# Kernel tuning notes

Hardware: AMD Instinct MI355X
Metric: run time of the kernel (lower is better)

Reference implementation:

```python
import jax, jax.numpy as jnp
import numpy as np

B, N, NODE_DIM = 64, 64, 192
H = 256          # node_hidden_dim
PDIM = 64        # property_embedding_dim
NUM_EDGE_TYPE = 5
T = 4            # message-passing rounds
E = 16384        # total edges (flattened batched graph)
E_SEL = 65536    # selected candidate pairs


def setup_inputs() -> dict:
    key = jax.random.key(0)
    ks = jax.random.split(key, 24)
    def g(k, shape, scale=0.05):
        return jax.random.normal(k, shape, dtype=jnp.float32) * scale
    inp = {
        "x": jax.random.normal(ks[0], (B, N, NODE_DIM), dtype=jnp.float32),
        "edge_index": jax.random.randint(ks[1], (2, E), 0, B * N, dtype=jnp.int32),
        "edge_attr": jax.random.uniform(ks[2], (E, NUM_EDGE_TYPE), dtype=jnp.float32),
        "props": jax.random.normal(ks[3], (B, 1), dtype=jnp.float32),
        "sel_b": jax.random.randint(ks[4], (E_SEL,), 0, B, dtype=jnp.int32),
        "sel_i": jax.random.randint(ks[5], (E_SEL,), 0, N, dtype=jnp.int32),
        "sel_j": jax.random.randint(ks[6], (E_SEL,), 0, N, dtype=jnp.int32),
        "golden_edge": jax.random.randint(ks[7], (E_SEL,), 0, NUM_EDGE_TYPE, dtype=jnp.int32),
        # parameters
        "W_prop": g(ks[8], (1, PDIM)), "b_prop": jnp.zeros((PDIM,), jnp.float32),
        "W_in": g(ks[9], (NODE_DIM, H)), "b_in": jnp.zeros((H,), jnp.float32),
        "W_msg": g(ks[10], (H + NUM_EDGE_TYPE, H)), "b_msg": jnp.zeros((H,), jnp.float32),
        "W_upd": g(ks[11], (2 * H, H)), "b_upd": jnp.zeros((H,), jnp.float32),
        "W_add": g(ks[12], (H + PDIM, H)), "b_add": jnp.zeros((H,), jnp.float32),
        "W1": g(ks[13], (2 * H, H)), "b1": jnp.zeros((H,), jnp.float32),
        "W2": g(ks[14], (H, H)), "b2": jnp.zeros((H,), jnp.float32),
        "W3": g(ks[15], (H, 2 * H)), "b3": jnp.zeros((2 * H,), jnp.float32),
        "W_out": g(ks[16], (2 * H, NUM_EDGE_TYPE)), "b_out": jnp.zeros((NUM_EDGE_TYPE,), jnp.float32),
    }
    return inp


def reference(x, edge_index, edge_attr, props, sel_b, sel_i, sel_j, golden_edge,
              W_prop, b_prop, W_in, b_in, W_msg, b_msg, W_upd, b_upd,
              W_add, b_add, W1, b1, W2, b2, W3, b3, W_out, b_out):
    BN = B * N
    node_x = x.reshape(BN, NODE_DIM)
    src, dst = edge_index[0], edge_index[1]

    # --- GNN node embedding (t rounds of message passing, opaque Encoder.embed_node) ---
    h = jax.nn.relu(node_x @ W_in + b_in)                       # [BN, H]
    for _ in range(T):
        msg_in = jnp.concatenate([h[src], edge_attr], axis=-1)  # [E, H+num_edge_type]
        msg = jax.nn.relu(msg_in @ W_msg + b_msg)               # [E, H]
        agg = jax.ops.segment_sum(msg, dst, num_segments=BN)    # [BN, H]
        h = jax.nn.relu(jnp.concatenate([h, agg], axis=-1) @ W_upd + b_upd)

    node_emb = h.reshape(B, N, H)

    # --- property conditioning + addition linear ---
    prop = props @ W_prop + b_prop                               # [B, PDIM]
    propp = jnp.broadcast_to(prop[:, None, :], (B, N, PDIM))
    node_embg = jnp.concatenate([node_emb, propp], axis=-1) @ W_add + b_add  # [B, N, H]

    # --- gather selected (src, dst) pairs directly (equiv. to repeat_interleave + boolean mask) ---
    flat = node_embg.reshape(BN, H)
    src_e = flat[sel_b * N + sel_i]                              # [E_SEL, H]
    dst_e = flat[sel_b * N + sel_j]                              # [E_SEL, H]
    pair = jnp.concatenate([src_e, dst_e], axis=-1)              # [E_SEL, 2H]

    # --- edge predictor MLP (3 layers, ReLU between) + output linear ---
    h1 = jax.nn.relu(pair @ W1 + b1)
    h2 = jax.nn.relu(h1 @ W2 + b2)
    h3 = h2 @ W3 + b3
    logits = h3 @ W_out + b_out                                  # [E_SEL, num_edge_type]

    # --- cross entropy (mean) ---
    logp = jax.nn.log_softmax(logits, axis=-1)
    loss = -jnp.mean(jnp.take_along_axis(logp, golden_edge[:, None].astype(jnp.int32), axis=-1))
    return loss
```

## Files before the change

### kernel.cpp

```cpp
#include <hip/hip_runtime.h>
#include <math.h>

#define BN 4096
#define N_PER_B 64
#define NE 16384
#define NSEL 65536
#define NET 5
#define PD 64
#define H1STR 260
#define FSTR 264
#define PTILES 2

typedef float f32x4 __attribute__((ext_vector_type(4)));
typedef float f32x16 __attribute__((ext_vector_type(16)));
typedef short short8 __attribute__((ext_vector_type(8)));
typedef short short4v __attribute__((ext_vector_type(4)));

__device__ __forceinline__ unsigned short f2bf(float f) {
    unsigned int u = __builtin_bit_cast(unsigned int, f);
    u += 0x7fff + ((u >> 16) & 1);
    return (unsigned short)(u >> 16);
}
__device__ __forceinline__ float bf_lo(unsigned int u) {
    return __builtin_bit_cast(float, u << 16);
}
__device__ __forceinline__ float bf_hi(unsigned int u) {
    return __builtin_bit_cast(float, u & 0xffff0000u);
}
__device__ __forceinline__ unsigned int pack2(float a, float b) {
    return (unsigned)f2bf(a) | ((unsigned)f2bf(b) << 16);
}
__device__ __forceinline__ short8 ld_frag(const unsigned short* p) {
    const short4v lo = *(const short4v*)(p);
    const short4v hi = *(const short4v*)(p + 4);
    return __builtin_shufflevector(lo, hi, 0, 1, 2, 3, 4, 5, 6, 7);
}
__device__ __forceinline__ unsigned int addrelu2(unsigned int a, unsigned int b, unsigned int c) {
    const float lo = fmaxf(bf_lo(a) + bf_lo(b) + bf_lo(c), 0.f);
    const float hi = fmaxf(bf_hi(a) + bf_hi(b) + bf_hi(c), 0.f);
    return pack2(lo, hi);
}

__global__ __launch_bounds__(256) void khist_rank(const int* __restrict__ eidx,
                                                  int* __restrict__ deg,
                                                  int* __restrict__ rank)
{
    const int e = blockIdx.x * 256 + threadIdx.x;
    rank[e] = atomicAdd(&deg[eidx[NE + e]], 1);
}

__global__ __launch_bounds__(256) void k_pre(
    const float* __restrict__ W_in, const float* __restrict__ W_msg,
    const float* __restrict__ W_upd, const float* __restrict__ W_add,
    const float* __restrict__ W1, const float* __restrict__ W2,
    const float* __restrict__ W3, const float* __restrict__ b3,
    const float* __restrict__ W_out, const float* __restrict__ b_out,
    const float* __restrict__ props, const float* __restrict__ W_prop,
    const float* __restrict__ b_prop, const float* __restrict__ b_add,
    const float* __restrict__ b_msg, const float* __restrict__ eattr,
    unsigned short* __restrict__ wbf, unsigned short* __restrict__ WfT,
    float* __restrict__ bfv, float* __restrict__ prop_add,
    unsigned short* __restrict__ ETc, float* __restrict__ out,
    int* __restrict__ deg)
{
    __shared__ __align__(16) char smem[16704];
    const int blk = blockIdx.x;
    const int tid = threadIdx.x;

    if (blk < 16) deg[blk * 256 + tid] = 0;
    if (blk == 0 && tid == 0) out[0] = 0.f;

    if (blk < 128) {
        float (*s)[65] = (float(*)[65])smem;
        const int wsel = blk >> 4;
        const int sub = blk & 15;
        const float* src; unsigned short* dst; int K = 256;
        switch (wsel) {
            case 0: src = W_in;              dst = wbf;                         K = 192; break;
            case 1: src = W_msg;             dst = wbf + 49152;                 break;
            case 2: src = W_upd;             dst = wbf + 49152 + 65536;         break;
            case 3: src = W_upd + 256 * 256; dst = wbf + 49152 + 2 * 65536;     break;
            case 4: src = W_add;             dst = wbf + 49152 + 3 * 65536;     break;
            case 5: src = W1;                dst = wbf + 49152 + 4 * 65536;     break;
            case 6: src = W1 + 256 * 256;    dst = wbf + 49152 + 5 * 65536;     break;
            default: src = W2;               dst = wbf + 49152 + 6 * 65536;     break;
        }
        const int k0 = (sub >> 2) * 64;
        const int n0 = (sub & 3) * 64;
        if (k0 >= K) return;
        const int tn = tid & 63;
        const int tg = tid >> 6;
        #pragma unroll
        for (int i = 0; i < 16; ++i) {
            const int kk = tg * 16 + i;
            s[kk][tn] = src[(size_t)(k0 + kk) * 256 + n0 + tn];
        }
        __syncthreads();
        #pragma unroll
        for (int i = 0; i < 16; ++i) {
            const int nn = tg * 16 + i;
            dst[(size_t)(n0 + nn) * K + k0 + tn] = f2bf(s[tn][nn]);
        }
    } else if (blk < 192) {
        const int b = blk - 128;
        const float pv = props[b];
        float acc = b_add[tid];
        for (int p = 0; p < PD; ++p) {
            const float e = fmaf(pv, W_prop[p], b_prop[p]);
            acc = fmaf(e, W_add[(256 + p) * 256 + tid], acc);
        }
        prop_add[b * 256 + tid] = acc;
    } else if (blk < 449) {
        float* part = (float*)smem;
        const int cb = blk - 192;
        float acc[NET] = {0.f, 0.f, 0.f, 0.f, 0.f};
        #pragma unroll
        for (int rep = 0; rep < 2; ++rep) {
            const int j = rep * 256 + tid;
            const float wv = (cb < 256) ? W3[(size_t)cb * 512 + j] : b3[j];
            #pragma unroll
            for (int t = 0; t < NET; ++t) acc[t] = fmaf(wv, W_out[j * NET + t], acc[t]);
        }
        #pragma unroll
        for (int t = 0; t < NET; ++t)
            for (int off = 32; off >= 1; off >>= 1) acc[t] += __shfl_down(acc[t], off);
        if ((tid & 63) == 0) {
            #pragma unroll
            for (int t = 0; t < NET; ++t) part[(tid >> 6) * NET + t] = acc[t];
        }
        __syncthreads();
        if (tid == 0) {
            float s[NET];
            #pragma unroll
            for (int t = 0; t < NET; ++t)
                s[t] = part[t] + part[NET + t] + part[2 * NET + t] + part[3 * NET + t];
            if (cb < 256) {
                #pragma unroll
                for (int t = 0; t < NET; ++t) WfT[t * 256 + cb] = f2bf(s[t]);
                #pragma unroll
                for (int t = NET; t < 16; ++t) WfT[t * 256 + cb] = 0;
            } else {
                #pragma unroll
                for (int t = 0; t < NET; ++t) bfv[t] = s[t] + b_out[t];
            }
        }
    } else {
        float* ea = (float*)smem;
        const int eb = (blk - 449) * 128;
        if (tid < 160)
            *(float4*)&ea[tid * 4] = *(const float4*)(eattr + (size_t)eb * 5 + tid * 4);
        __syncthreads();
        const float* Wme = W_msg + 256 * 256;
        const float w0 = Wme[0 * 256 + tid];
        const float w1 = Wme[1 * 256 + tid];
        const float w2 = Wme[2 * 256 + tid];
        const float w3 = Wme[3 * 256 + tid];
        const float w4 = Wme[4 * 256 + tid];
        const float bm = b_msg[tid];
        for (int i = 0; i < 128; ++i) {
            const float* a = ea + i * 5;
            float v = bm;
            v = fmaf(a[0], w0, v); v = fmaf(a[1], w1, v); v = fmaf(a[2], w2, v);
            v = fmaf(a[3], w3, v); v = fmaf(a[4], w4, v);
            ETc[(size_t)(eb + i) * 256 + tid] = f2bf(v);
        }
    }
}

__global__ __launch_bounds__(1024) void fstep(
    const float* __restrict__ x, const unsigned short* __restrict__ hbuf,
    const unsigned short* __restrict__ Pin, const unsigned short* __restrict__ ETc,
    const int* __restrict__ row_start, const int* __restrict__ srcs,
    const unsigned short* __restrict__ WaT, const unsigned short* __restrict__ WbT,
    const float* __restrict__ bias1,
    const unsigned short* __restrict__ Wp2T, const float* __restrict__ prop_add,
    const unsigned short* __restrict__ W1aT, const unsigned short* __restrict__ W1bT,
    unsigned short* __restrict__ hout, unsigned short* __restrict__ out1,
    unsigned short* __restrict__ out2, int mode,
    const int* __restrict__ eidx, const int* __restrict__ deg,
    const int* __restrict__ rank, int* __restrict__ srcs_w,
    int* __restrict__ row_start_w)
{
    __shared__ __align__(16) char smemb[4 * 16 * FSTR * 2];
    __shared__ int sEdge[256];
    unsigned short* Hg  = (unsigned short*)(smemb);
    unsigned short* Ag  = (unsigned short*)(smemb + 8448);
    unsigned short* Hs  = (unsigned short*)(smemb + 16896);
    unsigned short* H2s = (unsigned short*)(smemb + 25344);
    const int tid = threadIdx.x;

    if (mode == 0 && blockIdx.x >= 256) {
        int* sdeg = (int*)smemb;
        int* ssum = (int*)(smemb + 16384);
        const int t4 = tid * 4;
        const int4 v = *(const int4*)(deg + t4);
        const int l1 = v.x, l2 = v.x + v.y, l3 = v.x + v.y + v.z;
        ssum[tid] = l3 + v.w;
        __syncthreads();
        for (int off = 1; off < 1024; off <<= 1) {
            const int vv = ssum[tid];
            const int add = (tid >= off) ? ssum[tid - off] : 0;
            __syncthreads();
            ssum[tid] = vv + add;
            __syncthreads();
        }
        const int offset = (tid == 0) ? 0 : ssum[tid - 1];
        int4 rs;
        rs.x = offset; rs.y = offset + l1; rs.z = offset + l2; rs.w = offset + l3;
        *(int4*)(sdeg + t4) = rs;
        if (blockIdx.x == 256) {
            *(int4*)(row_start_w + t4) = rs;
            if (tid == 1023) row_start_w[4096] = NE;
        }
        __syncthreads();
        if (tid < 256) {
            const int e = (blockIdx.x - 256) * 256 + tid;
            const int d = eidx[NE + e];
            srcs_w[sdeg[d] + rank[e]] = eidx[e] | (e << 12);
        }
        return;
    }

    const int w = tid >> 6;
    const int lane = tid & 63;
    const int q = lane >> 4;
    const int tx = lane & 15;
    const int m0 = blockIdx.x * 16;
    const int col = w * 16 + tx;

    if (mode != 0) {
        {
            const int r = tid >> 6;
            const int c4 = (tid & 63) * 4;
            *(uint2*)(Hg + r * FSTR + c4) =
                *(const uint2*)(hbuf + (size_t)(m0 + r) * 256 + c4);
        }
        const int beg0 = row_start[m0];
        const int nE = row_start[m0 + 16] - beg0;
        const bool useLds = (nE <= 256);
        if (useLds && tid < nE) sEdge[tid] = srcs[beg0 + tid];
        __syncthreads();
        const int* ep = useLds ? (const int*)sEdge : srcs;
        const int ebias = useLds ? beg0 : 0;
        {
            const int node = m0 + w;
            const int beg = row_start[node] - ebias;
            const int end = row_start[node + 1] - ebias;
            const int c = lane * 4;
            float a0 = 0.f, a1 = 0.f, a2 = 0.f, a3 = 0.f;
            int idx = beg;
            for (; idx + 3 < end; idx += 4) {
                const int k0 = ep[idx],     k1 = ep[idx + 1];
                const int k2 = ep[idx + 2], k3 = ep[idx + 3];
                const uint2 p0 = *(const uint2*)(Pin + (size_t)(k0 & 4095) * 256 + c);
                const uint2 p1 = *(const uint2*)(Pin + (size_t)(k1 & 4095) * 256 + c);
                const uint2 p2 = *(const uint2*)(Pin + (size_t)(k2 & 4095) * 256 + c);
                const uint2 p3 = *(const uint2*)(Pin + (size_t)(k3 & 4095) * 256 + c);
                const uint2 e0 = *(const uint2*)(ETc + (size_t)(k0 >> 12) * 256 + c);
                const uint2 e1 = *(const uint2*)(ETc + (size_t)(k1 >> 12) * 256 + c);
                const uint2 e2 = *(const uint2*)(ETc + (size_t)(k2 >> 12) * 256 + c);
                const uint2 e3 = *(const uint2*)(ETc + (size_t)(k3 >> 12) * 256 + c);
                a0 += fmaxf(bf_lo(p0.x) + bf_lo(e0.x), 0.f) + fmaxf(bf_lo(p1.x) + bf_lo(e1.x), 0.f)
                    + fmaxf(bf_lo(p2.x) + bf_lo(e2.x), 0.f) + fmaxf(bf_lo(p3.x) + bf_lo(e3.x), 0.f);
                a1 += fmaxf(bf_hi(p0.x) + bf_hi(e0.x), 0.f) + fmaxf(bf_hi(p1.x) + bf_hi(e1.x), 0.f)
                    + fmaxf(bf_hi(p2.x) + bf_hi(e2.x), 0.f) + fmaxf(bf_hi(p3.x) + bf_hi(e3.x), 0.f);
                a2 += fmaxf(bf_lo(p0.y) + bf_lo(e0.y), 0.f) + fmaxf(bf_lo(p1.y) + bf_lo(e1.y), 0.f)
                    + fmaxf(bf_lo(p2.y) + bf_lo(e2.y), 0.f) + fmaxf(bf_lo(p3.y) + bf_lo(e3.y), 0.f);
                a3 += fmaxf(bf_hi(p0.y) + bf_hi(e0.y), 0.f) + fmaxf(bf_hi(p1.y) + bf_hi(e1.y), 0.f)
                    + fmaxf(bf_hi(p2.y) + bf_hi(e2.y), 0.f) + fmaxf(bf_hi(p3.y) + bf_hi(e3.y), 0.f);
            }
            for (; idx < end; ++idx) {
                const int pk = ep[idx];
                const uint2 pu = *(const uint2*)(Pin + (size_t)(pk & 4095) * 256 + c);
                const uint2 eu = *(const uint2*)(ETc + (size_t)(pk >> 12) * 256 + c);
                a0 += fmaxf(bf_lo(pu.x) + bf_lo(eu.x), 0.f);
                a1 += fmaxf(bf_hi(pu.x) + bf_hi(eu.x), 0.f);
                a2 += fmaxf(bf_lo(pu.y) + bf_lo(eu.y), 0.f);
                a3 += fmaxf(bf_hi(pu.y) + bf_hi(eu.y), 0.f);
            }
            uint2 o; o.x = pack2(a0, a1); o.y = pack2(a2, a3);
            *(uint2*)(Ag + w * FSTR + c) = o;
        }
        __syncthreads();
    }

    f32x4 acc = (f32x4)0.f;
    if (mode == 0) {
        #pragma unroll
        for (int s = 0; s < 6; ++s) {
            const int k0 = s * 32;
            const float* ap = x + (size_t)(m0 + tx) * 192 + k0 + q * 8;
            const float4 v0 = *(const float4*)ap;
            const float4 v1 = *(const float4*)(ap + 4);
            short8 af;
            af[0] = (short)f2bf(v0.x); af[1] = (short)f2bf(v0.y);
            af[2] = (short)f2bf(v0.z); af[3] = (short)f2bf(v0.w);
            af[4] = (short)f2bf(v1.x); af[5] = (short)f2bf(v1.y);
            af[6] = (short)f2bf(v1.z); af[7] = (short)f2bf(v1.w);
            const short8 bfr = *(const short8*)(WaT + (size_t)col * 192 + k0 + q * 8);
            acc = __builtin_amdgcn_mfma_f32_16x16x32_bf16(af, bfr, acc, 0, 0, 0);
        }
    } else {
        #pragma unroll
        for (int s = 0; s < 8; ++s) {
            const int k0 = s * 32;
            const short8 af = *(const short8*)(Hg + tx * FSTR + k0 + q * 8);
            const short8 bfr = *(const short8*)(WaT + (size_t)col * 256 + k0 + q * 8);
            acc = __builtin_amdgcn_mfma_f32_16x16x32_bf16(af, bfr, acc, 0, 0, 0);
        }
        #pragma unroll
        for (int s = 0; s < 8; ++s) {
            const int k0 = s * 32;
            const short8 af = *(const short8*)(Ag + tx * FSTR + k0 + q * 8);
            const short8 bfr = *(const short8*)(WbT + (size_t)col * 256 + k0 + q * 8);
            acc = __builtin_amdgcn_mfma_f32_16x16x32_bf16(af, bfr, acc, 0, 0, 0);
        }
    }
    {
        const float bv = bias1[col];
        #pragma unroll
        for (int r = 0; r < 4; ++r) {
            const int row = q * 4 + r;
            const unsigned short us = f2bf(fmaxf(acc[r] + bv, 0.f));
            Hs[row * FSTR + col] = us;
            if (mode < 2) hout[(size_t)(m0 + row) * 256 + col] = us;
        }
    }
    __syncthreads();

    acc = (f32x4)0.f;
    #pragma unroll
    for (int s = 0; s < 8; ++s) {
        const int k0 = s * 32;
        const short8 af = *(const short8*)(Hs + tx * FSTR + k0 + q * 8);
        const short8 bfr = *(const short8*)(Wp2T + (size_t)col * 256 + k0 + q * 8);
        acc = __builtin_amdgcn_mfma_f32_16x16x32_bf16(af, bfr, acc, 0, 0, 0);
    }
    if (mode < 2) {
        #pragma unroll
        for (int r = 0; r < 4; ++r)
            out1[(size_t)(m0 + q * 4 + r) * 256 + col] = f2bf(acc[r]);
        return;
    }
    {
        const float pv = prop_add[(m0 >> 6) * 256 + col];
        #pragma unroll
        for (int r = 0; r < 4; ++r)
            H2s[(q * 4 + r) * FSTR + col] = f2bf(acc[r] + pv);
    }
    __syncthreads();

    for (int which = 0; which < 2; ++which) {
        const unsigned short* WT = which ? W1bT : W1aT;
        unsigned short* op = which ? out2 : out1;
        acc = (f32x4)0.f;
        #pragma unroll
        for (int s = 0; s < 8; ++s) {
            const int k0 = s * 32;
            const short8 af = *(const short8*)(H2s + tx * FSTR + k0 + q * 8);
            const short8 bfr = *(const short8*)(WT + (size_t)col * 256 + k0 + q * 8);
            acc = __builtin_amdgcn_mfma_f32_16x16x32_bf16(af, bfr, acc, 0, 0, 0);
        }
        #pragma unroll
        for (int r = 0; r < 4; ++r)
            op[(size_t)(m0 + q * 4 + r) * 256 + col] = f2bf(acc[r]);
    }
}

__global__ __launch_bounds__(512, 2) void pair_k(
    const unsigned short* __restrict__ A1t, const unsigned short* __restrict__ A2t,
    const float* __restrict__ b1, const unsigned short* __restrict__ W2T,
    const float* __restrict__ b2, const unsigned short* __restrict__ WfT,
    const float* __restrict__ bfv,
    const int* __restrict__ sel_b, const int* __restrict__ sel_i,
    const int* __restrict__ sel_j, const int* __restrict__ golden,
    float* __restrict__ out)
{
    __shared__ __align__(16) unsigned short sbuf[64 * H1STR];
    __shared__ __align__(16) unsigned short b1s[256];
    __shared__ float Lg[64 * 8];
    __shared__ int sidx[64 * PTILES], didx[64 * PTILES], gold[64 * PTILES];

    const int tid = threadIdx.x;
    const int w = tid >> 6;
    const int lane = tid & 63;
    const int q = lane >> 4;
    const int tx = lane & 15;
    const int m = lane & 31;
    const int hh = lane >> 5;
    const int e0 = blockIdx.x * 64 * PTILES;

    if (tid < 64 * PTILES) {
        const int e = e0 + tid;
        const int b = sel_b[e];
        sidx[tid] = b * N_PER_B + sel_i[e];
        didx[tid] = b * N_PER_B + sel_j[e];
        gold[tid] = golden[e];
    }
    if (tid < 256) b1s[tid] = f2bf(b1[tid]);

    short8 Breg[16];
    {
        const unsigned short* bb = W2T + (size_t)(w * 32 + m) * 256 + hh * 8;
        #pragma unroll
        for (int s = 0; s < 16; ++s)
            Breg[s] = *(const short8*)(bb + s * 16);
    }
    __syncthreads();

    float total = 0.f;

    for (int t = 0; t < PTILES; ++t) {
        {
            const int hw = tid >> 5;
            #pragma unroll
            for (int j = 0; j < 4; ++j) {
                const int p = j * 16 + hw;
                const unsigned short* r1 = A1t + (size_t)sidx[t * 64 + p] * 256 + m * 8;
                const unsigned short* r2 = A2t + (size_t)didx[t * 64 + p] * 256 + m * 8;
                const uint4 u1 = *(const uint4*)r1;
                const uint4 u2 = *(const uint4*)r2;
                const uint4 ub = *(const uint4*)(b1s + m * 8);
                uint2 lo2, hi2;
                lo2.x = addrelu2(u1.x, u2.x, ub.x);
                lo2.y = addrelu2(u1.y, u2.y, ub.y);
                hi2.x = addrelu2(u1.z, u2.z, ub.z);
                hi2.y = addrelu2(u1.w, u2.w, ub.w);
                unsigned short* dbase = sbuf + p * H1STR + m * 8;
                *(uint2*)(dbase) = lo2;
                *(uint2*)(dbase + 4) = hi2;
            }
        }
        __syncthreads();

        f32x16 acc0 = (f32x16)0.f;
        f32x16 acc1 = (f32x16)0.f;
        {
            const unsigned short* a0row = sbuf + (size_t)m * H1STR + hh * 8;
            const unsigned short* a1row = a0row + 32 * H1STR;
            #pragma unroll
            for (int s = 0; s < 16; ++s) {
                const short8 af0 = ld_frag(a0row + s * 16);
                acc0 = __builtin_amdgcn_mfma_f32_32x32x16_bf16(af0, Breg[s], acc0, 0, 0, 0);
                const short8 af1 = ld_frag(a1row + s * 16);
                acc1 = __builtin_amdgcn_mfma_f32_32x32x16_bf16(af1, Breg[s], acc1, 0, 0, 0);
            }
        }
        __syncthreads();

        {
            const int col = w * 32 + m;
            const float bv = b2[col];
            #pragma unroll
            for (int reg = 0; reg < 16; ++reg) {
                const int prow = (reg & 3) + 8 * (reg >> 2) + 4 * hh;
                sbuf[prow * H1STR + col] = f2bf(fmaxf(acc0[reg] + bv, 0.f));
                sbuf[(32 + prow) * H1STR + col] = f2bf(fmaxf(acc1[reg] + bv, 0.f));
            }
        }
        __syncthreads();

        if (w < 4) {
            f32x4 accL = (f32x4)0.f;
            const unsigned short* a2row = sbuf + (size_t)(w * 16 + tx) * H1STR + q * 8;
            const unsigned short* bWf = WfT + (size_t)tx * 256 + q * 8;
            #pragma unroll
            for (int s = 0; s < 8; ++s) {
                const short8 af = ld_frag(a2row + s * 32);
                const short8 bfr = *(const short8*)(bWf + s * 32);
                accL = __builtin_amdgcn_mfma_f32_16x16x32_bf16(af, bfr, accL, 0, 0, 0);
            }
            if (tx < NET) {
                const float bb = bfv[tx];
                #pragma unroll
                for (int reg = 0; reg < 4; ++reg)
                    Lg[(w * 16 + q * 4 + reg) * 8 + tx] = accL[reg] + bb;
            }
        }
        __syncthreads();

        if (tid < 64) {
            float lg[NET];
            #pragma unroll
            for (int tt = 0; tt < NET; ++tt) lg[tt] = Lg[tid * 8 + tt];
            float mx = lg[0];
            #pragma unroll
            for (int tt = 1; tt < NET; ++tt) mx = fmaxf(mx, lg[tt]);
            float s = 0.f;
            #pragma unroll
            for (int tt = 0; tt < NET; ++tt) s += expf(lg[tt] - mx);
            float ls = mx + logf(s) - lg[gold[t * 64 + tid]];
            #pragma unroll
            for (int off = 32; off >= 1; off >>= 1) ls += __shfl_xor(ls, off);
            total += ls;
        }
        __syncthreads();
    }

    if (tid == 0) atomicAdd(out, total * (1.0f / NSEL));
}

extern "C" void kernel_launch(void* const* d_in, const int* in_sizes, int n_in,
                              void* d_out, int out_size, void* d_ws, size_t ws_size,
                              hipStream_t stream) {
    (void)in_sizes; (void)n_in; (void)out_size; (void)ws_size;
    const float* x      = (const float*)d_in[0];
    const int*   eidx   = (const int*)d_in[1];
    const float* eattr  = (const float*)d_in[2];
    const float* props  = (const float*)d_in[3];
    const int*   sel_b  = (const int*)d_in[4];
    const int*   sel_i  = (const int*)d_in[5];
    const int*   sel_j  = (const int*)d_in[6];
    const int*   golden = (const int*)d_in[7];
    const float* W_prop = (const float*)d_in[8];
    const float* b_prop = (const float*)d_in[9];
    const float* W_in   = (const float*)d_in[10];
    const float* b_in   = (const float*)d_in[11];
    const float* W_msg  = (const float*)d_in[12];
    const float* b_msg  = (const float*)d_in[13];
    const float* W_upd  = (const float*)d_in[14];
    const float* b_upd  = (const float*)d_in[15];
    const float* W_add  = (const float*)d_in[16];
    const float* b_add  = (const float*)d_in[17];
    const float* W1     = (const float*)d_in[18];
    const float* b1     = (const float*)d_in[19];
    const float* W2     = (const float*)d_in[20];
    const float* b2     = (const float*)d_in[21];
    const float* W3     = (const float*)d_in[22];
    const float* b3     = (const float*)d_in[23];
    const float* W_out  = (const float*)d_in[24];
    const float* b_out  = (const float*)d_in[25];

    const size_t SEG = (size_t)BN * 256;
    unsigned short* P0   = (unsigned short*)d_ws;
    unsigned short* P1   = P0 + SEG;
    unsigned short* hA   = P1 + SEG;
    unsigned short* hB   = hA + SEG;
    unsigned short* ETc  = hB + SEG;
    unsigned short* wbf  = ETc + (size_t)NE * 256;
    unsigned short* W_inT  = wbf;
    unsigned short* WmT    = wbf + 49152;
    unsigned short* WuaT   = WmT + 65536;
    unsigned short* WubT   = WuaT + 65536;
    unsigned short* W_addT = WubT + 65536;
    unsigned short* W1aT   = W_addT + 65536;
    unsigned short* W1bT   = W1aT + 65536;
    unsigned short* W2T    = W1bT + 65536;
    unsigned short* WfT    = W2T + 65536;
    float* prop_add = (float*)(WfT + 4096);
    float* bfv = prop_add + 64 * 256;
    int* row_start = (int*)(bfv + 16);
    int* srcs      = row_start + 4104;
    int* deg       = srcs + NE;
    int* rank      = deg + 4096;

    k_pre<<<577, 256, 0, stream>>>(W_in, W_msg, W_upd, W_add, W1, W2, W3, b3,
                                   W_out, b_out, props, W_prop, b_prop, b_add,
                                   b_msg, eattr, wbf, WfT, bfv, prop_add,
                                   ETc, (float*)d_out, deg);
    khist_rank<<<NE / 256, 256, 0, stream>>>(eidx, deg, rank);

    fstep<<<320, 1024, 0, stream>>>(x, nullptr, nullptr, ETc, row_start, srcs,
                                    W_inT, nullptr, b_in, WmT, nullptr, nullptr, nullptr,
                                    hA, P0, nullptr, 0,
                                    eidx, deg, rank, srcs, row_start);
    fstep<<<256, 1024, 0, stream>>>(nullptr, hA, P0, ETc, row_start, srcs,
                                    WuaT, WubT, b_upd, WmT, nullptr, nullptr, nullptr,
                                    hB, P1, nullptr, 1,
                                    nullptr, nullptr, nullptr, nullptr, nullptr);
    fstep<<<256, 1024, 0, stream>>>(nullptr, hB, P1, ETc, row_start, srcs,
                                    WuaT, WubT, b_upd, WmT, nullptr, nullptr, nullptr,
                                    hA, P0, nullptr, 1,
                                    nullptr, nullptr, nullptr, nullptr, nullptr);
    fstep<<<256, 1024, 0, stream>>>(nullptr, hA, P0, ETc, row_start, srcs,
                                    WuaT, WubT, b_upd, WmT, nullptr, nullptr, nullptr,
                                    hB, P1, nullptr, 1,
                                    nullptr, nullptr, nullptr, nullptr, nullptr);
    fstep<<<256, 1024, 0, stream>>>(nullptr, hB, P1, ETc, row_start, srcs,
                                    WuaT, WubT, b_upd, W_addT, prop_add, W1aT, W1bT,
                                    nullptr, P0, hA, 2,
                                    nullptr, nullptr, nullptr, nullptr, nullptr);

    pair_k<<<NSEL / (64 * PTILES), 512, 0, stream>>>(P0, hA, b1, W2T, b2, WfT, bfv,
                                    sel_b, sel_i, sel_j, golden, (float*)d_out);
}
```

Measured before the change: 240.3 us.

## Double-buffer pair tiles and overlap next-tile gather with output-layer MFMA

```diff
diff --git a/kernel.cpp b/kernel.cpp
--- a/kernel.cpp
+++ b/kernel.cpp
@@ -376,9 +376,9 @@
     const int* __restrict__ sel_j, const int* __restrict__ golden,
     float* __restrict__ out)
 {
-    __shared__ __align__(16) unsigned short sbuf[64 * H1STR];
+    __shared__ __align__(16) unsigned short sbuf[2][64 * H1STR];
     __shared__ __align__(16) unsigned short b1s[256];
-    __shared__ float Lg[64 * 8];
+    __shared__ float Lg[2][64 * 8];
     __shared__ int sidx[64 * PTILES], didx[64 * PTILES], gold[64 * PTILES];
 
     const int tid = threadIdx.x;
@@ -408,35 +408,56 @@
     }
     __syncthreads();
 
+    auto GATHER = [&](int tt, int bb, int tbase, int ngroups) {
+        const int hw = (tid - tbase) >> 5;
+        const int rounds = 64 / ngroups;
+        for (int j = 0; j < rounds; ++j) {
+            const int p = j * ngroups + hw;
+            const unsigned short* r1 = A1t + (size_t)sidx[tt * 64 + p] * 256 + m * 8;
+            const unsigned short* r2 = A2t + (size_t)didx[tt * 64 + p] * 256 + m * 8;
+            const uint4 u1 = *(const uint4*)r1;
+            const uint4 u2 = *(const uint4*)r2;
+            const uint4 ub = *(const uint4*)(b1s + m * 8);
+            uint2 lo2, hi2;
+            lo2.x = addrelu2(u1.x, u2.x, ub.x);
+            lo2.y = addrelu2(u1.y, u2.y, ub.y);
+            hi2.x = addrelu2(u1.z, u2.z, ub.z);
+            hi2.y = addrelu2(u1.w, u2.w, ub.w);
+            unsigned short* dbase = sbuf[bb] + p * H1STR + m * 8;
+            *(uint2*)(dbase) = lo2;
+            *(uint2*)(dbase + 4) = hi2;
+        }
+    };
+
     float total = 0.f;
+    auto CE = [&](int tt, int lb) {
+        float lg[NET];
+        #pragma unroll
+        for (int k = 0; k < NET; ++k) lg[k] = Lg[lb][tid * 8 + k];
+        float mx = lg[0];
+        #pragma unroll
+        for (int k = 1; k < NET; ++k) mx = fmaxf(mx, lg[k]);
+        float s = 0.f;
+        #pragma unroll
+        for (int k = 0; k < NET; ++k) s += expf(lg[k] - mx);
+        float ls = mx + logf(s) - lg[gold[tt * 64 + tid]];
+        #pragma unroll
+        for (int off = 32; off >= 1; off >>= 1) ls += __shfl_xor(ls, off);
+        total += ls;
+    };
+
+    GATHER(0, 0, 0, 16);
+    __syncthreads();
 
     for (int t = 0; t < PTILES; ++t) {
-        {
-            const int hw = tid >> 5;
-            #pragma unroll
-            for (int j = 0; j < 4; ++j) {
-                const int p = j * 16 + hw;
-                const unsigned short* r1 = A1t + (size_t)sidx[t * 64 + p] * 256 + m * 8;
-                const unsigned short* r2 = A2t + (size_t)didx[t * 64 + p] * 256 + m * 8;
-                const uint4 u1 = *(const uint4*)r1;
-                const uint4 u2 = *(const uint4*)r2;
-                const uint4 ub = *(const uint4*)(b1s + m * 8);
-                uint2 lo2, hi2;
-                lo2.x = addrelu2(u1.x, u2.x, ub.x);
-                lo2.y = addrelu2(u1.y, u2.y, ub.y);
-                hi2.x = addrelu2(u1.z, u2.z, ub.z);
-                hi2.y = addrelu2(u1.w, u2.w, ub.w);
-                unsigned short* dbase = sbuf + p * H1STR + m * 8;
-                *(uint2*)(dbase) = lo2;
-                *(uint2*)(dbase + 4) = hi2;
-            }
-        }
-        __syncthreads();
+        const int cb = t & 1;
+
+        if (t > 0 && tid < 64) CE(t - 1, (t - 1) & 1);
 
         f32x16 acc0 = (f32x16)0.f;
         f32x16 acc1 = (f32x16)0.f;
         {
-            const unsigned short* a0row = sbuf + (size_t)m * H1STR + hh * 8;
+            const unsigned short* a0row = sbuf[cb] + (size_t)m * H1STR + hh * 8;
             const unsigned short* a1row = a0row + 32 * H1STR;
             #pragma unroll
             for (int s = 0; s < 16; ++s) {
@@ -454,15 +475,15 @@
             #pragma unroll
             for (int reg = 0; reg < 16; ++reg) {
                 const int prow = (reg & 3) + 8 * (reg >> 2) + 4 * hh;
-                sbuf[prow * H1STR + col] = f2bf(fmaxf(acc0[reg] + bv, 0.f));
-                sbuf[(32 + prow) * H1STR + col] = f2bf(fmaxf(acc1[reg] + bv, 0.f));
+                sbuf[cb][prow * H1STR + col] = f2bf(fmaxf(acc0[reg] + bv, 0.f));
+                sbuf[cb][(32 + prow) * H1STR + col] = f2bf(fmaxf(acc1[reg] + bv, 0.f));
             }
         }
         __syncthreads();
 
         if (w < 4) {
             f32x4 accL = (f32x4)0.f;
-            const unsigned short* a2row = sbuf + (size_t)(w * 16 + tx) * H1STR + q * 8;
+            const unsigned short* a2row = sbuf[cb] + (size_t)(w * 16 + tx) * H1STR + q * 8;
             const unsigned short* bWf = WfT + (size_t)tx * 256 + q * 8;
             #pragma unroll
             for (int s = 0; s < 8; ++s) {
@@ -474,29 +495,15 @@
                 const float bb = bfv[tx];
                 #pragma unroll
                 for (int reg = 0; reg < 4; ++reg)
-                    Lg[(w * 16 + q * 4 + reg) * 8 + tx] = accL[reg] + bb;
-            }
-        }
-        __syncthreads();
-
-        if (tid < 64) {
-            float lg[NET];
-            #pragma unroll
-            for (int tt = 0; tt < NET; ++tt) lg[tt] = Lg[tid * 8 + tt];
-            float mx = lg[0];
-            #pragma unroll
-            for (int tt = 1; tt < NET; ++tt) mx = fmaxf(mx, lg[tt]);
-            float s = 0.f;
-            #pragma unroll
-            for (int tt = 0; tt < NET; ++tt) s += expf(lg[tt] - mx);
-            float ls = mx + logf(s) - lg[gold[t * 64 + tid]];
-            #pragma unroll
-            for (int off = 32; off >= 1; off >>= 1) ls += __shfl_xor(ls, off);
-            total += ls;
-        }
-        __syncthreads();
-    }
-
+                    Lg[cb][(w * 16 + q * 4 + reg) * 8 + tx] = accL[reg] + bb;
+            }
+        } else if (t + 1 < PTILES) {
+            GATHER(t + 1, (t + 1) & 1, 256, 8);
+        }
+        __syncthreads();
+    }
+
+    if (tid < 64) CE(PTILES - 1, (PTILES - 1) & 1);
     if (tid == 0) atomicAdd(out, total * (1.0f / NSEL));
 }
 
```

Measured after the change: 237.4 us (median of 2 runs). Within noise of the previous version (-1.2%).
